# Kernel optimization log

Hardware: AMD Instinct MI355X
Metric: run time of the kernel (lower is better)

The kernel has to match this reference:

```python
import jax, jax.numpy as jnp
import numpy as np

# 2nd-order Sobel kernels (kornia get_sobel_kernel2d_2nd_order): d2/dx2, d2/dxdy, d2/dy2
_KXX = np.array([[1., -2., 1.], [2., -4., 2.], [1., -2., 1.]], np.float32)
_KXY = np.array([[-1., 0., 1.], [0., 0., 0.], [1., 0., -1.]], np.float32)
_KERNELS = jnp.asarray(np.stack([_KXX, _KXY, _KXX.T])[:, None])  # (3,1,3,3)


def setup_inputs() -> dict:
    key = jax.random.key(0)
    x = jax.random.normal(key, (16, 3, 1024, 1024), dtype=jnp.float32)
    return {"x": x}


def reference(x):
    scale = 1.0
    B, C, H, W = x.shape
    # spatial_gradient_2nd_order: replicate pad + 3x3 conv per channel
    xp = jnp.pad(x.reshape(B * C, 1, H, W), ((0, 0), (0, 0), (1, 1), (1, 1)), mode='edge')
    g = jax.lax.conv_general_dilated(xp, _KERNELS, (1, 1), 'VALID')  # (B*C, 3, H, W)
    gxx, gxy, gyy = g[:, 0], g[:, 1], g[:, 2]
    # abs determinant of Hessian, clamp
    scores = jnp.abs(gxx * gyy - gxy * gxy) * (scale ** 4)
    scores = jnp.maximum(scores, 1e-6).reshape(B, C, H, W)
    # NMS via 3x3 max-pool (stride 1, SAME): keep only local maxima
    pooled = jax.lax.reduce_window(scores, -jnp.inf, jax.lax.max,
                                   (1, 1, 3, 3), (1, 1, 1, 1), 'SAME')
    scores = jnp.where(scores == pooled, scores, jnp.zeros((), scores.dtype))
    # global max normalization (adaptive_max_pool2d to 1x1)
    smax = jnp.max(scores, axis=(2, 3), keepdims=True)  # (B,C,1,1)
    return scores / smax
```

## Files before the change

### kernel.cpp

```cpp
#include <hip/hip_runtime.h>

#define H 1024
#define W 1024

__device__ __forceinline__ float score_ref(
    float a00, float a01, float a02,
    float a10, float a11, float a12,
    float a20, float a21, float a22)
{
#pragma clang fp contract(off)
    float gxx = a00;
    gxx = gxx - 2.0f * a01;
    gxx = gxx + a02;
    gxx = gxx + 2.0f * a10;
    gxx = gxx - 4.0f * a11;
    gxx = gxx + 2.0f * a12;
    gxx = gxx + a20;
    gxx = gxx - 2.0f * a21;
    gxx = gxx + a22;
    float gxy = -a00;
    gxy = gxy + a02;
    gxy = gxy + a20;
    gxy = gxy - a22;
    float gyy = a00;
    gyy = gyy + 2.0f * a01;
    gyy = gyy + a02;
    gyy = gyy - 2.0f * a10;
    gyy = gyy - 4.0f * a11;
    gyy = gyy - 2.0f * a12;
    gyy = gyy + a20;
    gyy = gyy + 2.0f * a21;
    gyy = gyy + a22;

    float p1 = gxx * gyy;
    float p2 = gxy * gxy;
    float det = p1 - p2;
    float s = fabsf(det);
    return s > 1e-6f ? s : 1e-6f;
}

__global__ __launch_bounds__(256) void hess_max_kernel(
    const float* __restrict__ x, unsigned int* __restrict__ pmax)
{
    const int plane = blockIdx.y;
    const int y0 = blockIdx.x * 32;
    const int t = threadIdx.x;
    const int c = t * 4;
    const float* px = x + (size_t)plane * H * W;

    float l0, l1, l2, r0, r1, r2;
    float4 m0, m1, m2;

    {
        int rr = y0 - 1 < 0 ? 0 : y0 - 1;
        const float* p = px + (size_t)rr * W;
        m0 = *(const float4*)(p + c);
        l0 = p[c == 0 ? 0 : c - 1];
        r0 = p[c + 4 >= W ? W - 1 : c + 4];
    }
    {
        const float* p = px + (size_t)y0 * W;
        m1 = *(const float4*)(p + c);
        l1 = p[c == 0 ? 0 : c - 1];
        r1 = p[c + 4 >= W ? W - 1 : c + 4];
    }

    float smax = 0.f;
    for (int y = y0; y < y0 + 32; ++y) {
        int rr = y + 1 >= H ? H - 1 : y + 1;
        const float* p = px + (size_t)rr * W;
        m2 = *(const float4*)(p + c);
        l2 = p[c == 0 ? 0 : c - 1];
        r2 = p[c + 4 >= W ? W - 1 : c + 4];

        float w0[6] = { l0, m0.x, m0.y, m0.z, m0.w, r0 };
        float w1[6] = { l1, m1.x, m1.y, m1.z, m1.w, r1 };
        float w2[6] = { l2, m2.x, m2.y, m2.z, m2.w, r2 };
#pragma unroll
        for (int j = 0; j < 4; ++j) {
            float s = score_ref(w0[j], w0[j+1], w0[j+2],
                                w1[j], w1[j+1], w1[j+2],
                                w2[j], w2[j+1], w2[j+2]);
            smax = fmaxf(smax, s);
        }
        m0 = m1; l0 = l1; r0 = r1;
        m1 = m2; l1 = l2; r1 = r2;
    }

#pragma unroll
    for (int off = 32; off > 0; off >>= 1)
        smax = fmaxf(smax, __shfl_down(smax, off));
    if ((t & 63) == 0)
        atomicMax(pmax + plane, __float_as_uint(smax));
}

#define TW 64
#define TH 16
#define IW 68
#define IH 20
#define SW 66
#define SH 18
__global__ __launch_bounds__(256) void hess_out_kernel(
    const float* __restrict__ x, const unsigned int* __restrict__ pmax,
    float* __restrict__ out)
{
    __shared__ float lin[IH * IW];
    __shared__ float ls[SH * SW];
    const int plane = blockIdx.z;
    const int x0 = blockIdx.x * TW;
    const int y0 = blockIdx.y * TH;
    const int t = threadIdx.x;
    const float* px = x + (size_t)plane * H * W;

    for (int i = t; i < IH * IW; i += 256) {
        int r = i / IW, cc = i % IW;
        int gy = y0 - 2 + r; gy = gy < 0 ? 0 : (gy >= H ? H - 1 : gy);
        int gx = x0 - 2 + cc; gx = gx < 0 ? 0 : (gx >= W ? W - 1 : gx);
        lin[i] = px[(size_t)gy * W + gx];
    }
    __syncthreads();

    for (int i = t; i < SH * SW; i += 256) {
        int sy = i / SW, sx = i % SW;
        int gy = y0 - 1 + sy, gx = x0 - 1 + sx;
        float v = 0.f;
        if (gy >= 0 && gy < H && gx >= 0 && gx < W) {
            const float* p0 = &lin[sy * IW + sx];
            v = score_ref(p0[0], p0[1], p0[2],
                          p0[IW], p0[IW + 1], p0[IW + 2],
                          p0[2 * IW], p0[2 * IW + 1], p0[2 * IW + 2]);
        }
        ls[i] = v;
    }
    __syncthreads();

    const float smax = __uint_as_float(pmax[plane]);
    const int ox = t & 63;
    const int oyb = t >> 6;
#pragma unroll
    for (int k = 0; k < 4; ++k) {
        int oy = oyb * 4 + k;
        const float* p = &ls[oy * SW + ox];
        float s = p[SW + 1];
        float m = fmaxf(fmaxf(fmaxf(p[0], p[1]), fmaxf(p[2], p[SW])),
                        fmaxf(fmaxf(p[SW + 1], p[SW + 2]),
                              fmaxf(fmaxf(p[2 * SW], p[2 * SW + 1]), p[2 * SW + 2])));
        float v = (s == m) ? s / smax : 0.f;
        out[(size_t)plane * H * W + (size_t)(y0 + oy) * W + (x0 + ox)] = v;
    }
}

extern "C" void kernel_launch(void* const* d_in, const int* in_sizes, int n_in,
                              void* d_out, int out_size, void* d_ws, size_t ws_size,
                              hipStream_t stream) {
    const float* x = (const float*)d_in[0];
    float* out = (float*)d_out;
    unsigned int* pmax = (unsigned int*)d_ws;
    const int planes = in_sizes[0] / (H * W);

    hipMemsetAsync(pmax, 0, planes * sizeof(unsigned int), stream);

    dim3 g1(H / 32, planes);
    hess_max_kernel<<<g1, 256, 0, stream>>>(x, pmax);

    dim3 g2(W / TW, H / TH, planes);
    hess_out_kernel<<<g2, 256, 0, stream>>>(x, pmax, out);
}
```

Baseline: 474.5 us.

## Materialize Hessian scores in workspace and run NMS from stored scores

The first pass now writes the per-pixel determinant-of-Hessian scores to a workspace buffer while it computes the per-plane max. The second pass loads those scores into shared memory instead of recomputing the 3x3 convolutions from the input. It also uses a wider tile, float4 stores and multiplication by a reciprocal instead of division. The aim is to cut redundant arithmetic and halo recomputation, at the cost of an extra full-size write and read of the score buffer. The original two-kernel path is kept as a fallback when the workspace is too small.

```diff
diff --git a/kernel.cpp b/kernel.cpp
--- a/kernel.cpp
+++ b/kernel.cpp
@@ -2,6 +2,7 @@
 
 #define H 1024
 #define W 1024
+#define HW (H * W)
 
 __device__ __forceinline__ float score_ref(
     float a00, float a01, float a02,
@@ -9,27 +10,24 @@
     float a20, float a21, float a22)
 {
 #pragma clang fp contract(off)
-    float gxx = a00;
-    gxx = gxx - 2.0f * a01;
+    float gxx = fmaf(-2.0f, a01, a00);
     gxx = gxx + a02;
-    gxx = gxx + 2.0f * a10;
-    gxx = gxx - 4.0f * a11;
-    gxx = gxx + 2.0f * a12;
+    gxx = fmaf(2.0f, a10, gxx);
+    gxx = fmaf(-4.0f, a11, gxx);
+    gxx = fmaf(2.0f, a12, gxx);
     gxx = gxx + a20;
-    gxx = gxx - 2.0f * a21;
+    gxx = fmaf(-2.0f, a21, gxx);
     gxx = gxx + a22;
-    float gxy = -a00;
-    gxy = gxy + a02;
+    float gxy = a02 - a00;
     gxy = gxy + a20;
     gxy = gxy - a22;
-    float gyy = a00;
-    gyy = gyy + 2.0f * a01;
+    float gyy = fmaf(2.0f, a01, a00);
     gyy = gyy + a02;
-    gyy = gyy - 2.0f * a10;
-    gyy = gyy - 4.0f * a11;
-    gyy = gyy - 2.0f * a12;
+    gyy = fmaf(-2.0f, a10, gyy);
+    gyy = fmaf(-4.0f, a11, gyy);
+    gyy = fmaf(-2.0f, a12, gyy);
     gyy = gyy + a20;
-    gyy = gyy + 2.0f * a21;
+    gyy = fmaf(2.0f, a21, gyy);
     gyy = gyy + a22;
 
     float p1 = gxx * gyy;
@@ -39,14 +37,17 @@
     return s > 1e-6f ? s : 1e-6f;
 }
 
-__global__ __launch_bounds__(256) void hess_max_kernel(
-    const float* __restrict__ x, unsigned int* __restrict__ pmax)
+
+__global__ __launch_bounds__(256) void hess_score_max_kernel(
+    const float* __restrict__ x, float* __restrict__ sc,
+    unsigned int* __restrict__ pmax)
 {
     const int plane = blockIdx.y;
     const int y0 = blockIdx.x * 32;
     const int t = threadIdx.x;
     const int c = t * 4;
-    const float* px = x + (size_t)plane * H * W;
+    const float* px = x + (size_t)plane * HW;
+    float* psc = sc + (size_t)plane * HW;
 
     float l0, l1, l2, r0, r1, r2;
     float4 m0, m1, m2;
@@ -76,13 +77,15 @@
         float w0[6] = { l0, m0.x, m0.y, m0.z, m0.w, r0 };
         float w1[6] = { l1, m1.x, m1.y, m1.z, m1.w, r1 };
         float w2[6] = { l2, m2.x, m2.y, m2.z, m2.w, r2 };
+        float s[4];
 #pragma unroll
         for (int j = 0; j < 4; ++j) {
-            float s = score_ref(w0[j], w0[j+1], w0[j+2],
-                                w1[j], w1[j+1], w1[j+2],
-                                w2[j], w2[j+1], w2[j+2]);
-            smax = fmaxf(smax, s);
+            s[j] = score_ref(w0[j], w0[j+1], w0[j+2],
+                             w1[j], w1[j+1], w1[j+2],
+                             w2[j], w2[j+1], w2[j+2]);
+            smax = fmaxf(smax, s[j]);
         }
+        *(float4*)(psc + (size_t)y * W + c) = make_float4(s[0], s[1], s[2], s[3]);
         m0 = m1; l0 = l1; r0 = r1;
         m1 = m2; l1 = l2; r1 = r2;
     }
@@ -94,59 +97,157 @@
         atomicMax(pmax + plane, __float_as_uint(smax));
 }
 
-#define TW 64
+#define TW 128
 #define TH 16
-#define IW 68
-#define IH 20
-#define SW 66
+#define SW 132
 #define SH 18
-__global__ __launch_bounds__(256) void hess_out_kernel(
-    const float* __restrict__ x, const unsigned int* __restrict__ pmax,
+__global__ __launch_bounds__(256) void hess_nms_kernel(
+    const float* __restrict__ sc, const unsigned int* __restrict__ pmax,
     float* __restrict__ out)
 {
-    __shared__ float lin[IH * IW];
     __shared__ float ls[SH * SW];
     const int plane = blockIdx.z;
     const int x0 = blockIdx.x * TW;
     const int y0 = blockIdx.y * TH;
     const int t = threadIdx.x;
-    const float* px = x + (size_t)plane * H * W;
-
-    for (int i = t; i < IH * IW; i += 256) {
-        int r = i / IW, cc = i % IW;
+    const float* ps = sc + (size_t)plane * HW;
+
+    for (int i = t; i < SH * SW; i += 256) {
+        int sy = i / SW, sx = i - sy * SW;
+        int gy = y0 - 1 + sy, gx = x0 - 1 + sx;
+        float v = 0.f;
+        if (gy >= 0 && gy < H && gx >= 0 && gx < W)
+            v = ps[(size_t)gy * W + gx];
+        ls[i] = v;
+    }
+    __syncthreads();
+
+    const float inv = 1.0f / __uint_as_float(pmax[plane]);
+    const int cc = (t & 31) * 4;
+    const int r0 = t >> 5;
+    float* po = out + (size_t)plane * HW;
+
+#pragma unroll
+    for (int k = 0; k < 2; ++k) {
+        const int r = r0 + k * 8;
+        const float* b0 = &ls[(r + 0) * SW + cc];
+        const float* b1 = &ls[(r + 1) * SW + cc];
+        const float* b2 = &ls[(r + 2) * SW + cc];
+        float4 o;
+        float* ov = (float*)&o;
+#pragma unroll
+        for (int j = 0; j < 4; ++j) {
+            float s = b1[j + 1];
+            float m = fmaxf(fmaxf(fmaxf(b0[j], b0[j+1]), fmaxf(b0[j+2], b1[j])),
+                            fmaxf(fmaxf(b1[j+1], b1[j+2]),
+                                  fmaxf(fmaxf(b2[j], b2[j+1]), b2[j+2])));
+            ov[j] = (s == m) ? s * inv : 0.f;
+        }
+        *(float4*)(po + (size_t)(y0 + r) * W + (x0 + cc)) = o;
+    }
+}
+
+
+__global__ __launch_bounds__(256) void hess_max_fb(
+    const float* __restrict__ x, unsigned int* __restrict__ pmax)
+{
+    const int plane = blockIdx.y;
+    const int y0 = blockIdx.x * 32;
+    const int t = threadIdx.x;
+    const int c = t * 4;
+    const float* px = x + (size_t)plane * HW;
+
+    float l0, l1, l2, r0, r1, r2;
+    float4 m0, m1, m2;
+    {
+        int rr = y0 - 1 < 0 ? 0 : y0 - 1;
+        const float* p = px + (size_t)rr * W;
+        m0 = *(const float4*)(p + c);
+        l0 = p[c == 0 ? 0 : c - 1];
+        r0 = p[c + 4 >= W ? W - 1 : c + 4];
+    }
+    {
+        const float* p = px + (size_t)y0 * W;
+        m1 = *(const float4*)(p + c);
+        l1 = p[c == 0 ? 0 : c - 1];
+        r1 = p[c + 4 >= W ? W - 1 : c + 4];
+    }
+    float smax = 0.f;
+    for (int y = y0; y < y0 + 32; ++y) {
+        int rr = y + 1 >= H ? H - 1 : y + 1;
+        const float* p = px + (size_t)rr * W;
+        m2 = *(const float4*)(p + c);
+        l2 = p[c == 0 ? 0 : c - 1];
+        r2 = p[c + 4 >= W ? W - 1 : c + 4];
+        float w0[6] = { l0, m0.x, m0.y, m0.z, m0.w, r0 };
+        float w1[6] = { l1, m1.x, m1.y, m1.z, m1.w, r1 };
+        float w2[6] = { l2, m2.x, m2.y, m2.z, m2.w, r2 };
+#pragma unroll
+        for (int j = 0; j < 4; ++j)
+            smax = fmaxf(smax, score_ref(w0[j], w0[j+1], w0[j+2],
+                                         w1[j], w1[j+1], w1[j+2],
+                                         w2[j], w2[j+1], w2[j+2]));
+        m0 = m1; l0 = l1; r0 = r1;
+        m1 = m2; l1 = l2; r1 = r2;
+    }
+#pragma unroll
+    for (int off = 32; off > 0; off >>= 1)
+        smax = fmaxf(smax, __shfl_down(smax, off));
+    if ((t & 63) == 0)
+        atomicMax(pmax + plane, __float_as_uint(smax));
+}
+
+#define FTW 64
+#define FTH 16
+#define FIW 68
+#define FIH 20
+#define FSW 66
+#define FSH 18
+__global__ __launch_bounds__(256) void hess_out_fb(
+    const float* __restrict__ x, const unsigned int* __restrict__ pmax,
+    float* __restrict__ out)
+{
+    __shared__ float lin[FIH * FIW];
+    __shared__ float ls[FSH * FSW];
+    const int plane = blockIdx.z;
+    const int x0 = blockIdx.x * FTW;
+    const int y0 = blockIdx.y * FTH;
+    const int t = threadIdx.x;
+    const float* px = x + (size_t)plane * HW;
+
+    for (int i = t; i < FIH * FIW; i += 256) {
+        int r = i / FIW, cc = i % FIW;
         int gy = y0 - 2 + r; gy = gy < 0 ? 0 : (gy >= H ? H - 1 : gy);
         int gx = x0 - 2 + cc; gx = gx < 0 ? 0 : (gx >= W ? W - 1 : gx);
         lin[i] = px[(size_t)gy * W + gx];
     }
     __syncthreads();
-
-    for (int i = t; i < SH * SW; i += 256) {
-        int sy = i / SW, sx = i % SW;
+    for (int i = t; i < FSH * FSW; i += 256) {
+        int sy = i / FSW, sx = i % FSW;
         int gy = y0 - 1 + sy, gx = x0 - 1 + sx;
         float v = 0.f;
         if (gy >= 0 && gy < H && gx >= 0 && gx < W) {
-            const float* p0 = &lin[sy * IW + sx];
+            const float* p0 = &lin[sy * FIW + sx];
             v = score_ref(p0[0], p0[1], p0[2],
-                          p0[IW], p0[IW + 1], p0[IW + 2],
-                          p0[2 * IW], p0[2 * IW + 1], p0[2 * IW + 2]);
+                          p0[FIW], p0[FIW + 1], p0[FIW + 2],
+                          p0[2 * FIW], p0[2 * FIW + 1], p0[2 * FIW + 2]);
         }
         ls[i] = v;
     }
     __syncthreads();
-
-    const float smax = __uint_as_float(pmax[plane]);
+    const float inv = 1.0f / __uint_as_float(pmax[plane]);
     const int ox = t & 63;
     const int oyb = t >> 6;
 #pragma unroll
     for (int k = 0; k < 4; ++k) {
         int oy = oyb * 4 + k;
-        const float* p = &ls[oy * SW + ox];
-        float s = p[SW + 1];
-        float m = fmaxf(fmaxf(fmaxf(p[0], p[1]), fmaxf(p[2], p[SW])),
-                        fmaxf(fmaxf(p[SW + 1], p[SW + 2]),
-                              fmaxf(fmaxf(p[2 * SW], p[2 * SW + 1]), p[2 * SW + 2])));
-        float v = (s == m) ? s / smax : 0.f;
-        out[(size_t)plane * H * W + (size_t)(y0 + oy) * W + (x0 + ox)] = v;
+        const float* p = &ls[oy * FSW + ox];
+        float s = p[FSW + 1];
+        float m = fmaxf(fmaxf(fmaxf(p[0], p[1]), fmaxf(p[2], p[FSW])),
+                        fmaxf(fmaxf(p[FSW + 1], p[FSW + 2]),
+                              fmaxf(fmaxf(p[2 * FSW], p[2 * FSW + 1]), p[2 * FSW + 2])));
+        float v = (s == m) ? s * inv : 0.f;
+        out[(size_t)plane * HW + (size_t)(y0 + oy) * W + (x0 + ox)] = v;
     }
 }
 
@@ -155,14 +256,28 @@
                               hipStream_t stream) {
     const float* x = (const float*)d_in[0];
     float* out = (float*)d_out;
-    unsigned int* pmax = (unsigned int*)d_ws;
-    const int planes = in_sizes[0] / (H * W);
-
-    hipMemsetAsync(pmax, 0, planes * sizeof(unsigned int), stream);
-
-    dim3 g1(H / 32, planes);
-    hess_max_kernel<<<g1, 256, 0, stream>>>(x, pmax);
-
-    dim3 g2(W / TW, H / TH, planes);
-    hess_out_kernel<<<g2, 256, 0, stream>>>(x, pmax, out);
-}
+    const int planes = in_sizes[0] / HW;
+
+    const size_t sc_bytes = (size_t)planes * HW * sizeof(float);
+
+    if (ws_size >= sc_bytes + planes * sizeof(unsigned int)) {
+        float* sc = (float*)d_ws;
+        unsigned int* pmax = (unsigned int*)((char*)d_ws + sc_bytes);
+        hipMemsetAsync(pmax, 0, planes * sizeof(unsigned int), stream);
+
+        dim3 g1(H / 32, planes);
+        hess_score_max_kernel<<<g1, 256, 0, stream>>>(x, sc, pmax);
+
+        dim3 g2(W / TW, H / TH, planes);
+        hess_nms_kernel<<<g2, 256, 0, stream>>>(sc, pmax, out);
+    } else {
+        unsigned int* pmax = (unsigned int*)d_ws;
+        hipMemsetAsync(pmax, 0, planes * sizeof(unsigned int), stream);
+
+        dim3 g1(H / 32, planes);
+        hess_max_fb<<<g1, 256, 0, stream>>>(x, pmax);
+
+        dim3 g2(W / FTW, H / FTH, planes);
+        hess_out_fb<<<g2, 256, 0, stream>>>(x, pmax, out);
+    }
+}
```

Result: no change. 475.0 us (+0.1%).

## Restructure Hessian NMS as register-streamed row strips with separable max pass

Applied to the files above, without the earlier changes.

The NMS/output kernel drops its shared-memory tiles. Each thread now owns four columns of a 16-row strip and streams rows through registers, keeping three score rows for the 3x3 max and storing results as float4. The max pass uses a separable Sobel decomposition with FMAs and a prefetch of the next row, and both kernels use a smaller strip size for more blocks. The separable arithmetic in the max pass changes rounding, so the global max may differ slightly from the exact score values used in the NMS pass, which risks small normalization mismatches.

```diff
diff --git a/kernel.cpp b/kernel.cpp
--- a/kernel.cpp
+++ b/kernel.cpp
@@ -2,6 +2,8 @@
 
 #define H 1024
 #define W 1024
+#define HW (H * W)
+#define STRIP 16
 
 __device__ __forceinline__ float score_ref(
     float a00, float a01, float a02,
@@ -9,27 +11,24 @@
     float a20, float a21, float a22)
 {
 #pragma clang fp contract(off)
-    float gxx = a00;
-    gxx = gxx - 2.0f * a01;
+    float gxx = fmaf(-2.0f, a01, a00);
     gxx = gxx + a02;
-    gxx = gxx + 2.0f * a10;
-    gxx = gxx - 4.0f * a11;
-    gxx = gxx + 2.0f * a12;
+    gxx = fmaf(2.0f, a10, gxx);
+    gxx = fmaf(-4.0f, a11, gxx);
+    gxx = fmaf(2.0f, a12, gxx);
     gxx = gxx + a20;
-    gxx = gxx - 2.0f * a21;
+    gxx = fmaf(-2.0f, a21, gxx);
     gxx = gxx + a22;
-    float gxy = -a00;
-    gxy = gxy + a02;
+    float gxy = a02 - a00;
     gxy = gxy + a20;
     gxy = gxy - a22;
-    float gyy = a00;
-    gyy = gyy + 2.0f * a01;
+    float gyy = fmaf(2.0f, a01, a00);
     gyy = gyy + a02;
-    gyy = gyy - 2.0f * a10;
-    gyy = gyy - 4.0f * a11;
-    gyy = gyy - 2.0f * a12;
+    gyy = fmaf(-2.0f, a10, gyy);
+    gyy = fmaf(-4.0f, a11, gyy);
+    gyy = fmaf(-2.0f, a12, gyy);
     gyy = gyy + a20;
-    gyy = gyy + 2.0f * a21;
+    gyy = fmaf(2.0f, a21, gyy);
     gyy = gyy + a22;
 
     float p1 = gxx * gyy;
@@ -39,52 +38,63 @@
     return s > 1e-6f ? s : 1e-6f;
 }
 
+struct Row8 { float a[8]; };
+
+__device__ __forceinline__ Row8 load_row8(const float* __restrict__ prow, int c, int t)
+{
+    const float4 m = *(const float4*)(prow + c);
+    int lc = c - 2; lc = lc < 0 ? 0 : lc;
+    const float2 L = *(const float2*)(prow + lc);
+    int rc = c + 4; rc = rc > (W - 2) ? (W - 2) : rc;
+    const float2 R = *(const float2*)(prow + rc);
+    float l0 = L.x, l1 = L.y;
+    if (t == 0) l1 = L.x;
+    float q0 = R.x, q1 = R.y;
+    if (t == 255) q0 = R.y;
+    Row8 r;
+    r.a[0] = l0; r.a[1] = l1;
+    r.a[2] = m.x; r.a[3] = m.y; r.a[4] = m.z; r.a[5] = m.w;
+    r.a[6] = q0; r.a[7] = q1;
+    return r;
+}
+
 __global__ __launch_bounds__(256) void hess_max_kernel(
     const float* __restrict__ x, unsigned int* __restrict__ pmax)
 {
     const int plane = blockIdx.y;
-    const int y0 = blockIdx.x * 32;
+    const int y0 = blockIdx.x * STRIP;
     const int t = threadIdx.x;
     const int c = t * 4;
-    const float* px = x + (size_t)plane * H * W;
+    const float* px = x + (size_t)plane * HW;
 
-    float l0, l1, l2, r0, r1, r2;
-    float4 m0, m1, m2;
+    Row8 r0 = load_row8(px + (size_t)(y0 - 1 < 0 ? 0 : y0 - 1) * W, c, t);
+    Row8 r1 = load_row8(px + (size_t)y0 * W, c, t);
+    Row8 r2 = load_row8(px + (size_t)(y0 + 1 > H - 1 ? H - 1 : y0 + 1) * W, c, t);
+    Row8 r3 = load_row8(px + (size_t)(y0 + 2 > H - 1 ? H - 1 : y0 + 2) * W, c, t);
 
-    {
-        int rr = y0 - 1 < 0 ? 0 : y0 - 1;
-        const float* p = px + (size_t)rr * W;
-        m0 = *(const float4*)(p + c);
-        l0 = p[c == 0 ? 0 : c - 1];
-        r0 = p[c + 4 >= W ? W - 1 : c + 4];
-    }
-    {
-        const float* p = px + (size_t)y0 * W;
-        m1 = *(const float4*)(p + c);
-        l1 = p[c == 0 ? 0 : c - 1];
-        r1 = p[c + 4 >= W ? W - 1 : c + 4];
-    }
+    float smax = 1e-6f;
+#pragma unroll
+    for (int i = 0; i < STRIP; ++i) {
+        const int sy = y0 + i;
+        const int pf = sy + 3 > H - 1 ? H - 1 : sy + 3;
+        Row8 r4 = load_row8(px + (size_t)pf * W, c, t);
 
-    float smax = 0.f;
-    for (int y = y0; y < y0 + 32; ++y) {
-        int rr = y + 1 >= H ? H - 1 : y + 1;
-        const float* p = px + (size_t)rr * W;
-        m2 = *(const float4*)(p + c);
-        l2 = p[c == 0 ? 0 : c - 1];
-        r2 = p[c + 4 >= W ? W - 1 : c + 4];
-
-        float w0[6] = { l0, m0.x, m0.y, m0.z, m0.w, r0 };
-        float w1[6] = { l1, m1.x, m1.y, m1.z, m1.w, r1 };
-        float w2[6] = { l2, m2.x, m2.y, m2.z, m2.w, r2 };
+        float P[6], Q[6], Rv[6];
+#pragma unroll
+        for (int k = 0; k < 6; ++k) {
+            P[k] = fmaf(2.0f, r1.a[k + 1], r0.a[k + 1]) + r2.a[k + 1];
+            Q[k] = fmaf(-2.0f, r1.a[k + 1], r0.a[k + 1]) + r2.a[k + 1];
+            Rv[k] = r0.a[k + 1] - r2.a[k + 1];
+        }
 #pragma unroll
         for (int j = 0; j < 4; ++j) {
-            float s = score_ref(w0[j], w0[j+1], w0[j+2],
-                                w1[j], w1[j+1], w1[j+2],
-                                w2[j], w2[j+1], w2[j+2]);
-            smax = fmaxf(smax, s);
+            float gxx = fmaf(-2.0f, P[j + 1], P[j]) + P[j + 2];
+            float gyy = fmaf(2.0f, Q[j + 1], Q[j]) + Q[j + 2];
+            float gxy = Rv[j + 2] - Rv[j];
+            float det = fmaf(gxx, gyy, -(gxy * gxy));
+            smax = fmaxf(smax, fabsf(det));
         }
-        m0 = m1; l0 = l1; r0 = r1;
-        m1 = m2; l1 = l2; r1 = r2;
+        r0 = r1; r1 = r2; r2 = r3; r3 = r4;
     }
 
 #pragma unroll
@@ -94,59 +104,68 @@
         atomicMax(pmax + plane, __float_as_uint(smax));
 }
 
-#define TW 64
-#define TH 16
-#define IW 68
-#define IH 20
-#define SW 66
-#define SH 18
-__global__ __launch_bounds__(256) void hess_out_kernel(
+struct S6 { float s[6]; };
+
+__device__ __forceinline__ S6 score_row_exact(const Row8& A, const Row8& B, const Row8& C)
+{
+    S6 o;
+#pragma unroll
+    for (int i = 0; i < 6; ++i)
+        o.s[i] = score_ref(A.a[i], A.a[i + 1], A.a[i + 2],
+                           B.a[i], B.a[i + 1], B.a[i + 2],
+                           C.a[i], C.a[i + 1], C.a[i + 2]);
+    return o;
+}
+
+__global__ __launch_bounds__(256) void hess_nms_kernel(
     const float* __restrict__ x, const unsigned int* __restrict__ pmax,
     float* __restrict__ out)
 {
-    __shared__ float lin[IH * IW];
-    __shared__ float ls[SH * SW];
-    const int plane = blockIdx.z;
-    const int x0 = blockIdx.x * TW;
-    const int y0 = blockIdx.y * TH;
+    const int plane = blockIdx.y;
+    const int y0 = blockIdx.x * STRIP;
     const int t = threadIdx.x;
-    const float* px = x + (size_t)plane * H * W;
+    const int c = t * 4;
+    const float* px = x + (size_t)plane * HW;
+    float* po = out + (size_t)plane * HW;
+    const float inv = 1.0f / __uint_as_float(pmax[plane]);
 
-    for (int i = t; i < IH * IW; i += 256) {
-        int r = i / IW, cc = i % IW;
-        int gy = y0 - 2 + r; gy = gy < 0 ? 0 : (gy >= H ? H - 1 : gy);
-        int gx = x0 - 2 + cc; gx = gx < 0 ? 0 : (gx >= W ? W - 1 : gx);
-        lin[i] = px[(size_t)gy * W + gx];
-    }
-    __syncthreads();
+    Row8 rm2 = load_row8(px + (size_t)(y0 - 2 < 0 ? 0 : y0 - 2) * W, c, t);
+    Row8 r0  = load_row8(px + (size_t)(y0 - 1 < 0 ? 0 : y0 - 1) * W, c, t);
+    Row8 r1  = load_row8(px + (size_t)y0 * W, c, t);
+    Row8 r2  = load_row8(px + (size_t)(y0 + 1 > H - 1 ? H - 1 : y0 + 1) * W, c, t);
+    Row8 r3  = load_row8(px + (size_t)(y0 + 2 > H - 1 ? H - 1 : y0 + 2) * W, c, t);
 
-    for (int i = t; i < SH * SW; i += 256) {
-        int sy = i / SW, sx = i % SW;
-        int gy = y0 - 1 + sy, gx = x0 - 1 + sx;
-        float v = 0.f;
-        if (gy >= 0 && gy < H && gx >= 0 && gx < W) {
-            const float* p0 = &lin[sy * IW + sx];
-            v = score_ref(p0[0], p0[1], p0[2],
-                          p0[IW], p0[IW + 1], p0[IW + 2],
-                          p0[2 * IW], p0[2 * IW + 1], p0[2 * IW + 2]);
+    S6 zero;
+#pragma unroll
+    for (int i = 0; i < 6; ++i) zero.s[i] = 0.0f;
+
+    S6 sp = zero;
+    if (y0 > 0) sp = score_row_exact(rm2, r0, r1);
+    S6 sc_ = score_row_exact(r0, r1, r2);
+
+#pragma unroll
+    for (int i = 0; i < STRIP; ++i) {
+        const int sy = y0 + i;
+        const int pf = sy + 3 > H - 1 ? H - 1 : sy + 3;
+        Row8 r4 = load_row8(px + (size_t)pf * W, c, t);
+
+        S6 sn = zero;
+        if (sy + 1 < H) sn = score_row_exact(r1, r2, r3);
+
+        float4 o;
+        float* ov = (float*)&o;
+#pragma unroll
+        for (int j = 0; j < 4; ++j) {
+            float s = sc_.s[j + 1];
+            float m = fmaxf(fmaxf(fmaxf(sp.s[j], sp.s[j + 1]), fmaxf(sp.s[j + 2], sc_.s[j])),
+                            fmaxf(fmaxf(sc_.s[j + 1], sc_.s[j + 2]),
+                                  fmaxf(fmaxf(sn.s[j], sn.s[j + 1]), sn.s[j + 2])));
+            ov[j] = (s == m) ? s * inv : 0.0f;
         }
-        ls[i] = v;
-    }
-    __syncthreads();
+        *(float4*)(po + (size_t)sy * W + c) = o;
 
-    const float smax = __uint_as_float(pmax[plane]);
-    const int ox = t & 63;
-    const int oyb = t >> 6;
-#pragma unroll
-    for (int k = 0; k < 4; ++k) {
-        int oy = oyb * 4 + k;
-        const float* p = &ls[oy * SW + ox];
-        float s = p[SW + 1];
-        float m = fmaxf(fmaxf(fmaxf(p[0], p[1]), fmaxf(p[2], p[SW])),
-                        fmaxf(fmaxf(p[SW + 1], p[SW + 2]),
-                              fmaxf(fmaxf(p[2 * SW], p[2 * SW + 1]), p[2 * SW + 2])));
-        float v = (s == m) ? s / smax : 0.f;
-        out[(size_t)plane * H * W + (size_t)(y0 + oy) * W + (x0 + ox)] = v;
+        r0 = r1; r1 = r2; r2 = r3; r3 = r4;
+        sp = sc_; sc_ = sn;
     }
 }
 
@@ -156,13 +175,11 @@
     const float* x = (const float*)d_in[0];
     float* out = (float*)d_out;
     unsigned int* pmax = (unsigned int*)d_ws;
-    const int planes = in_sizes[0] / (H * W);
+    const int planes = in_sizes[0] / HW;
 
     hipMemsetAsync(pmax, 0, planes * sizeof(unsigned int), stream);
 
-    dim3 g1(H / 32, planes);
-    hess_max_kernel<<<g1, 256, 0, stream>>>(x, pmax);
-
-    dim3 g2(W / TW, H / TH, planes);
-    hess_out_kernel<<<g2, 256, 0, stream>>>(x, pmax, out);
+    dim3 grid(H / STRIP, planes);
+    hess_max_kernel<<<grid, 256, 0, stream>>>(x, pmax);
+    hess_nms_kernel<<<grid, 256, 0, stream>>>(x, pmax, out);
 }
```

Measured after the change: 422.8 us. 10.9% less time.
